# Optimization experiments

Hardware: AMD Instinct MI355X
Metric: run time of the kernel (lower is better)

Reference implementation:

```python
import jax, jax.numpy as jnp
import numpy as np

NUM_HEADS = 16


def setup_inputs() -> dict:
    key = jax.random.key(0)
    ks = jax.random.split(key, 7)
    B, N, D = 16, 512, 1024
    return {
        "x": jax.random.normal(ks[0], (B, N, D), dtype=jnp.float32),
        "spatial_encoding": jax.random.normal(ks[1], (B, N, N), dtype=jnp.float32),
        "edge_encoding": jax.random.normal(ks[2], (B, N, N), dtype=jnp.float32),
        "Wq": jax.random.normal(ks[3], (D, D), dtype=jnp.float32) * (D ** -0.5),
        "Wk": jax.random.normal(ks[4], (D, D), dtype=jnp.float32) * (D ** -0.5),
        "Wv": jax.random.normal(ks[5], (D, D), dtype=jnp.float32) * (D ** -0.5),
        "Wo": jax.random.normal(ks[6], (D, D), dtype=jnp.float32) * (D ** -0.5),
    }


def reference(x, spatial_encoding, edge_encoding, Wq, Wk, Wv, Wo):
    B, N, D = x.shape
    H = NUM_HEADS
    hd = D // H
    scale = D ** -0.5  # NOTE: source scales by hidden_dim**-0.5, not head_size**-0.5

    def split_heads(t):  # (B,N,D) -> (B,H,N,hd)
        return t.reshape(B, N, H, hd).transpose(0, 2, 1, 3)

    q = split_heads(x @ Wq.T)
    k = split_heads(x @ Wk.T)
    v = split_heads(x @ Wv.T)

    bias = (spatial_encoding + edge_encoding)[:, None]  # (B,1,N,N)
    a = jnp.einsum("bhnd,bhmd->bhnm", q, k) * scale + bias  # (B,H,N,N)

    # rows that are entirely zero (padded) are masked to -inf
    row_nonzero = jnp.any(a != 0, axis=-1, keepdims=True)  # (B,H,N,1)
    a = jnp.where(row_nonzero, a, -jnp.inf)
    p = jax.nn.softmax(a, axis=-1)
    p = jnp.where(jnp.isnan(p), 0.0, p)  # nan_to_num after softmax of all -inf rows

    o = jnp.einsum("bhnm,bhmd->bhnd", p, v)  # (B,H,N,hd)
    o = o.transpose(0, 2, 1, 3).reshape(B, N, D)
    return o @ Wo.T
```

## Files before the change

### kernel.cpp

```cpp
#include <hip/hip_runtime.h>
#include <cstdint>


typedef unsigned short u16;
typedef unsigned int   u32;
typedef __attribute__((ext_vector_type(8))) short bf8;
typedef __attribute__((ext_vector_type(4))) float f4;

__device__ __forceinline__ u16 f2bf(float x) {
  u32 u = __float_as_uint(x);
  u += 0x7FFF + ((u >> 16) & 1);
  return (u16)(u >> 16);
}

__device__ __forceinline__ float bf2f(u16 x) {
  return __uint_as_float(((u32)x) << 16);
}

__device__ __forceinline__ void gl2lds16(const void* g, void* l) {
  __builtin_amdgcn_global_load_lds(
      (const __attribute__((address_space(1))) u32*)g,
      (__attribute__((address_space(3))) u32*)l, 16, 0, 0);
}


__global__ __launch_bounds__(256) void cast_bf16(const float* __restrict__ src,
                                                 uint4* __restrict__ dst, int n8) {
  const int i = blockIdx.x * 256 + threadIdx.x;
  if (i >= n8) return;
  const float4* s = (const float4*)src;
  const float4 a = s[2 * i], c = s[2 * i + 1];
  uint4 o;
  o.x = (u32)f2bf(a.x) | ((u32)f2bf(a.y) << 16);
  o.y = (u32)f2bf(a.z) | ((u32)f2bf(a.w) << 16);
  o.z = (u32)f2bf(c.x) | ((u32)f2bf(c.y) << 16);
  o.w = (u32)f2bf(c.z) | ((u32)f2bf(c.w) << 16);
  dst[i] = o;
}

__global__ __launch_bounds__(256) void cast4_bf16(
    const float* __restrict__ s0, const float* __restrict__ s1,
    const float* __restrict__ s2, const float* __restrict__ s3,
    uint4* __restrict__ d0, uint4* __restrict__ d1,
    uint4* __restrict__ d2, uint4* __restrict__ d3) {
  const int i = blockIdx.x * 256 + threadIdx.x;
  const int w = i >> 17, j = i & 131071;
  const float* src = (w == 0) ? s0 : (w == 1) ? s1 : (w == 2) ? s2 : s3;
  uint4* dst = (w == 0) ? d0 : (w == 1) ? d1 : (w == 2) ? d2 : d3;
  const float4* s = (const float4*)src;
  const float4 a = s[2 * j], c = s[2 * j + 1];
  uint4 o;
  o.x = (u32)f2bf(a.x) | ((u32)f2bf(a.y) << 16);
  o.y = (u32)f2bf(a.z) | ((u32)f2bf(a.w) << 16);
  o.z = (u32)f2bf(c.x) | ((u32)f2bf(c.y) << 16);
  o.w = (u32)f2bf(c.z) | ((u32)f2bf(c.w) << 16);
  dst[j] = o;
}

__global__ __launch_bounds__(256) void bias_perm(const float* __restrict__ sp,
                                                 const float* __restrict__ ed,
                                                 u16* __restrict__ Bp) {
  const int jt = blockIdx.x, qt = blockIdx.y, b = blockIdx.z;
  const int tid = threadIdx.x;
  const int wave = tid >> 6, quad = (tid >> 4) & 3, l16 = tid & 15;
  const int qrl = (wave << 4) + (quad << 2);
  union { u16 a[16]; uint4 v[2]; } tmp;
#pragma unroll
  for (int nb = 0; nb < 4; nb++) {
    const int col = (jt << 6) + (nb << 4) + l16;
#pragma unroll
    for (int r = 0; r < 4; r++) {
      const int row = (qt << 6) + qrl + r;
      const size_t idx = ((size_t)b << 18) + (size_t)row * 512 + col;
      tmp.a[nb * 4 + r] = f2bf(sp[idx] + ed[idx]);
    }
  }
  uint4* out = (uint4*)Bp + ((((size_t)b * 8 + qt) * 8 + jt) * 256 + tid) * 2;
  out[0] = tmp.v[0];
  out[1] = tmp.v[1];
}


__device__ __forceinline__ void gemm_core(const u16* __restrict__ A,
                                          const u16* __restrict__ Bt,
                                          int m0, int n0,
                                          u16* lA, u16* lB, f4 acc[4][4]) {
  const int tid  = threadIdx.x;
  const int wave = tid >> 6;
  const int lane = tid & 63;
  const int quad = lane >> 4;
  const int l16  = lane & 15;
  const int wm   = (wave >> 1) << 6;
  const int wn   = (wave & 1) << 6;
  const int srow = tid >> 3;
  const int scol = ((tid & 7) ^ (srow & 7)) << 3;
  const int c0   = (quad ^ (l16 & 7)) << 3;

  f4 zero = {0.f, 0.f, 0.f, 0.f};
#pragma unroll
  for (int mi = 0; mi < 4; mi++)
#pragma unroll
    for (int ni = 0; ni < 4; ni++) acc[mi][ni] = zero;

  const u16* Ab = A  + (size_t)(m0 + srow) * 1024 + scol;
  const u16* Bb = Bt + (size_t)(n0 + srow) * 1024 + scol;

  for (int k0 = 0; k0 < 1024; k0 += 64) {
    __syncthreads();
#pragma unroll
    for (int i = 0; i < 4; i++) {
      gl2lds16(Ab + (size_t)(i << 5) * 1024 + k0,
               (char*)lA + (((i << 8) + (wave << 6)) << 4));
      gl2lds16(Bb + (size_t)(i << 5) * 1024 + k0,
               (char*)lB + (((i << 8) + (wave << 6)) << 4));
    }
    __syncthreads();
#pragma unroll
    for (int kk = 0; kk < 64; kk += 32) {
      const int o = c0 ^ kk;
      bf8 af[4], bfr[4];
#pragma unroll
      for (int mi = 0; mi < 4; mi++)
        af[mi] = *(const bf8*)(lA + (wm + (mi << 4) + l16) * 64 + o);
#pragma unroll
      for (int ni = 0; ni < 4; ni++)
        bfr[ni] = *(const bf8*)(lB + (wn + (ni << 4) + l16) * 64 + o);
#pragma unroll
      for (int mi = 0; mi < 4; mi++)
#pragma unroll
        for (int ni = 0; ni < 4; ni++)
          acc[mi][ni] = __builtin_amdgcn_mfma_f32_16x16x32_bf16(
              af[mi], bfr[ni], acc[mi][ni], 0, 0, 0);
    }
  }
}


__global__ __launch_bounds__(256) void qkv_kernel(
    const u16* __restrict__ xb, const u16* __restrict__ wq,
    const u16* __restrict__ wk, const u16* __restrict__ wv,
    u16* __restrict__ Qh, u16* __restrict__ Kh, u16* __restrict__ Vt) {
  __shared__ __align__(16) u16 lA[128 * 64];
  __shared__ __align__(16) u16 lB[128 * 64];
  const int flat = blockIdx.x + (blockIdx.y << 3) + (blockIdx.z << 9);
  const int m_tile = (flat & 7) | (((flat >> 6) & 7) << 3);
  const int n_tile = (flat >> 3) & 7;
  const int proj = flat >> 9;
  const int m0 = m_tile << 7, n0 = n_tile << 7;
  const u16* W = (proj == 0) ? wq : (proj == 1) ? wk : wv;
  f4 acc[4][4];
  gemm_core(xb, W, m0, n0, lA, lB, acc);

  const int tid = threadIdx.x, wave = tid >> 6, lane = tid & 63;
  const int quad = lane >> 4, l16 = lane & 15;
  const int wm = (wave >> 1) << 6, wn = (wave & 1) << 6;

  if (proj == 2) {
#pragma unroll
    for (int mi = 0; mi < 4; mi++) {
      const int gmb = m0 + wm + (mi << 4) + (quad << 2);
      const int b = gmb >> 9, nb = gmb & 511;
#pragma unroll
      for (int ni = 0; ni < 4; ni++) {
        const int gn = n0 + wn + (ni << 4) + l16;
        const int h = gn >> 6, hdi = gn & 63;
        ushort4 pk;
        pk.x = f2bf(acc[mi][ni][0]);
        pk.y = f2bf(acc[mi][ni][1]);
        pk.z = f2bf(acc[mi][ni][2]);
        pk.w = f2bf(acc[mi][ni][3]);
        *(ushort4*)(Vt + ((size_t)((b << 4) + h) * 64 + hdi) * 512 + nb) = pk;
      }
    }
  } else {
    u16* dst = (proj == 0) ? Qh : Kh;
#pragma unroll
    for (int mi = 0; mi < 4; mi++) {
#pragma unroll
      for (int r = 0; r < 4; r++) {
        const int gm = m0 + wm + (mi << 4) + (quad << 2) + r;
        const int b = gm >> 9, n = gm & 511;
#pragma unroll
        for (int ni = 0; ni < 4; ni++) {
          const int gn = n0 + wn + (ni << 4) + l16;
          const int h = gn >> 6, hdi = gn & 63;
          dst[((size_t)((b << 4) + h) * 512 + n) * 64 + hdi] = f2bf(acc[mi][ni][r]);
        }
      }
    }
  }
}


__global__ __launch_bounds__(256) void oproj_kernel(const u16* __restrict__ Ob,
                                                    const u16* __restrict__ wo,
                                                    float* __restrict__ out) {
  __shared__ __align__(16) u16 lA[128 * 64];
  __shared__ __align__(16) u16 lB[128 * 64];
  const int flat = blockIdx.x + (blockIdx.y << 3);
  const int m0 = ((flat & 7) | (((flat >> 6) & 7) << 3)) << 7;
  const int n0 = ((flat >> 3) & 7) << 7;
  f4 acc[4][4];
  gemm_core(Ob, wo, m0, n0, lA, lB, acc);

  const int tid = threadIdx.x, wave = tid >> 6, lane = tid & 63;
  const int quad = lane >> 4, l16 = lane & 15;
  const int wm = (wave >> 1) << 6, wn = (wave & 1) << 6;
#pragma unroll
  for (int mi = 0; mi < 4; mi++)
#pragma unroll
    for (int r = 0; r < 4; r++) {
      const int gm = m0 + wm + (mi << 4) + (quad << 2) + r;
#pragma unroll
      for (int ni = 0; ni < 4; ni++) {
        const int gn = n0 + wn + (ni << 4) + l16;
        out[(size_t)gm * 1024 + gn] = acc[mi][ni][r];
      }
    }
}


__global__ __launch_bounds__(256) void attn_kernel(
    const u16* __restrict__ Qh, const u16* __restrict__ Kh,
    const u16* __restrict__ Vt, const u16* __restrict__ Bp,
    u16* __restrict__ Ob) {
  __shared__ __align__(16) u16 sQ[64 * 64];
  __shared__ __align__(16) u16 sK[64 * 64];
  __shared__ __align__(16) u16 sV[64 * 64];
  __shared__ __align__(16) u16 sP[4 * 16 * 72];
  const int flat = blockIdx.x + (blockIdx.y << 3) + (blockIdx.z << 7);
  const int qt = (flat >> 3) & 7;
  const int h  = (flat >> 6) & 15;
  const int b  = (flat & 7) | (((flat >> 10) & 1) << 3);
  const int q0 = qt << 6;
  const int tid = threadIdx.x, wave = tid >> 6, lane = tid & 63;
  const int quad = lane >> 4, l16 = lane & 15;
  const int c0  = (quad ^ (l16 & 7)) << 3;
  const int swb = (((tid & 7) ^ ((tid >> 3) & 7)) << 4);

  const u16* Qg = Qh + ((size_t)((b << 4) + h) * 512 + q0) * 64;
  const u16* Kg = Kh + (size_t)((b << 4) + h) * 512 * 64;
  const u16* Vg = Vt + (size_t)((b << 4) + h) * 64 * 512;
  const uint4* Bpg = (const uint4*)Bp + (((size_t)b * 8 + qt) * 8 * 256 + tid) * 2;

#pragma unroll
  for (int i = 0; i < 2; i++) {
    const int e = (i << 8) + tid;
    gl2lds16((const char*)Qg + (e >> 3) * 128 + swb,
             (char*)sQ + (((i << 8) + (wave << 6)) << 4));
  }

  f4 o[4];
  f4 zero = {0.f, 0.f, 0.f, 0.f};
#pragma unroll
  for (int i = 0; i < 4; i++) o[i] = zero;
  float lsum[4] = {0.f, 0.f, 0.f, 0.f};
  const int qrl = (wave << 4) + (quad << 2);

  for (int j0 = 0; j0 < 512; j0 += 64) {
    const uint4 bc0 = Bpg[(j0 >> 6) * 512];
    const uint4 bc1 = Bpg[(j0 >> 6) * 512 + 1];
    const u32 bw[8] = {bc0.x, bc0.y, bc0.z, bc0.w, bc1.x, bc1.y, bc1.z, bc1.w};

    __syncthreads();
#pragma unroll
    for (int i = 0; i < 2; i++) {
      const int e = (i << 8) + tid;
      gl2lds16((const char*)Kg + (size_t)j0 * 128 + (e >> 3) * 128 + swb,
               (char*)sK + (((i << 8) + (wave << 6)) << 4));
      gl2lds16((const char*)Vg + (size_t)(e >> 3) * 1024 + j0 * 2 + swb,
               (char*)sV + (((i << 8) + (wave << 6)) << 4));
    }
    __syncthreads();

    bf8 aq0 = *(const bf8*)(sQ + ((wave << 4) + l16) * 64 + c0);
    bf8 aq1 = *(const bf8*)(sQ + ((wave << 4) + l16) * 64 + (c0 ^ 32));
    u16* pw = sP + wave * (16 * 72);
#pragma unroll
    for (int nb = 0; nb < 4; nb++) {
      bf8 b0 = *(const bf8*)(sK + ((nb << 4) + l16) * 64 + c0);
      bf8 b1 = *(const bf8*)(sK + ((nb << 4) + l16) * 64 + (c0 ^ 32));
      f4 s = zero;
      s = __builtin_amdgcn_mfma_f32_16x16x32_bf16(aq0, b0, s, 0, 0, 0);
      s = __builtin_amdgcn_mfma_f32_16x16x32_bf16(aq1, b1, s, 0, 0, 0);
#pragma unroll
      for (int r = 0; r < 4; r++) {
        const u32 w = bw[nb * 2 + (r >> 1)];
        const float bias = bf2f((r & 1) ? (u16)(w >> 16) : (u16)(w & 0xFFFF));
        const float ev = __expf(s[r] * 0.03125f + bias);
        lsum[r] += ev;
        pw[((quad << 2) + r) * 72 + (nb << 4) + l16] = f2bf(ev);
      }
    }

    bf8 ap0 = *(const bf8*)(pw + l16 * 72 + (quad << 3));
    bf8 ap1 = *(const bf8*)(pw + l16 * 72 + 32 + (quad << 3));
#pragma unroll
    for (int db = 0; db < 4; db++) {
      bf8 v0 = *(const bf8*)(sV + ((db << 4) + l16) * 64 + c0);
      bf8 v1 = *(const bf8*)(sV + ((db << 4) + l16) * 64 + (c0 ^ 32));
      o[db] = __builtin_amdgcn_mfma_f32_16x16x32_bf16(ap0, v0, o[db], 0, 0, 0);
      o[db] = __builtin_amdgcn_mfma_f32_16x16x32_bf16(ap1, v1, o[db], 0, 0, 0);
    }
  }

#pragma unroll
  for (int r = 0; r < 4; r++) {
    float s = lsum[r];
    s += __shfl_xor(s, 1);
    s += __shfl_xor(s, 2);
    s += __shfl_xor(s, 4);
    s += __shfl_xor(s, 8);
    const float inv = 1.f / s;
    const int gr = q0 + qrl + r;
#pragma unroll
    for (int db = 0; db < 4; db++)
      Ob[(size_t)((b << 9) + gr) * 1024 + (h << 6) + (db << 4) + l16] =
          f2bf(o[db][r] * inv);
  }
}


extern "C" void kernel_launch(void* const* d_in, const int* in_sizes, int n_in,
                              void* d_out, int out_size, void* d_ws, size_t ws_size,
                              hipStream_t stream) {
  const float* x  = (const float*)d_in[0];
  const float* sp = (const float*)d_in[1];
  const float* ed = (const float*)d_in[2];
  const float* Wq = (const float*)d_in[3];
  const float* Wk = (const float*)d_in[4];
  const float* Wv = (const float*)d_in[5];
  const float* Wo = (const float*)d_in[6];
  float* out = (float*)d_out;

  char* w = (char*)d_ws;
  u16* xb  = (u16*)(w);
  u16* wqb = (u16*)(w + 16777216);
  u16* wkb = (u16*)(w + 18874368);
  u16* wvb = (u16*)(w + 20971520);
  u16* wob = (u16*)(w + 23068672);
  u16* Qh  = (u16*)(w + 25165824);
  u16* Kh  = (u16*)(w + 41943040);
  u16* Vt  = (u16*)(w + 58720256);
  u16* Ob  = (u16*)(w + 75497472);
  u16* Bp  = (u16*)(w + 92274688);

  cast_bf16<<<4096, 256, 0, stream>>>(x, (uint4*)xb, 1048576);
  cast4_bf16<<<2048, 256, 0, stream>>>(Wq, Wk, Wv, Wo,
                                       (uint4*)wqb, (uint4*)wkb,
                                       (uint4*)wvb, (uint4*)wob);
  bias_perm<<<dim3(8, 8, 16), 256, 0, stream>>>(sp, ed, Bp);

  qkv_kernel<<<dim3(8, 64, 3), 256, 0, stream>>>(xb, wqb, wkb, wvb, Qh, Kh, Vt);
  attn_kernel<<<dim3(8, 16, 16), 256, 0, stream>>>(Qh, Kh, Vt, Bp, Ob);
  oproj_kernel<<<dim3(8, 64, 1), 256, 0, stream>>>(Ob, wob, out);
}
```

Measured before the change: 251.7 us.

## Keep softmax probabilities in registers via transposed QK^T and fp16 PV MFMA

The attention kernel now computes S^T (K as the A operand, Q as B) so that each lane's exp values directly form the B operand of a 16x16x16 fp16 MFMA for P·V. This removes the per-wave LDS staging buffer for P and its write/read round trip. V is now stored as fp16 instead of bf16 so the PV MFMA can use fp16 inputs. The bias permutation is changed to match the transposed layout. The three prep kernels are merged into one launch. The fp16 P and V trade range for mantissa precision, and the PV product now issues more, smaller MFMAs.

```diff
diff --git a/kernel.cpp b/kernel.cpp
--- a/kernel.cpp
+++ b/kernel.cpp
@@ -5,6 +5,7 @@
 typedef unsigned short u16;
 typedef unsigned int   u32;
 typedef __attribute__((ext_vector_type(8))) short bf8;
+typedef __attribute__((ext_vector_type(4))) _Float16 h4;
 typedef __attribute__((ext_vector_type(4))) float f4;
 
 __device__ __forceinline__ u16 f2bf(float x) {
@@ -17,6 +18,12 @@
   return __uint_as_float(((u32)x) << 16);
 }
 
+__device__ __forceinline__ u16 f2h(float x) {
+  union { _Float16 h; u16 u; } c;
+  c.h = (_Float16)x;
+  return c.u;
+}
+
 __device__ __forceinline__ void gl2lds16(const void* g, void* l) {
   __builtin_amdgcn_global_load_lds(
       (const __attribute__((address_space(1))) u32*)g,
@@ -24,60 +31,57 @@
 }
 
 
-__global__ __launch_bounds__(256) void cast_bf16(const float* __restrict__ src,
-                                                 uint4* __restrict__ dst, int n8) {
-  const int i = blockIdx.x * 256 + threadIdx.x;
-  if (i >= n8) return;
-  const float4* s = (const float4*)src;
-  const float4 a = s[2 * i], c = s[2 * i + 1];
-  uint4 o;
-  o.x = (u32)f2bf(a.x) | ((u32)f2bf(a.y) << 16);
-  o.y = (u32)f2bf(a.z) | ((u32)f2bf(a.w) << 16);
-  o.z = (u32)f2bf(c.x) | ((u32)f2bf(c.y) << 16);
-  o.w = (u32)f2bf(c.z) | ((u32)f2bf(c.w) << 16);
-  dst[i] = o;
-}
-
-__global__ __launch_bounds__(256) void cast4_bf16(
-    const float* __restrict__ s0, const float* __restrict__ s1,
-    const float* __restrict__ s2, const float* __restrict__ s3,
+__global__ __launch_bounds__(256) void prep_kernel(
+    const float* __restrict__ x, const float* __restrict__ sp,
+    const float* __restrict__ ed,
+    const float* __restrict__ W0, const float* __restrict__ W1,
+    const float* __restrict__ W2, const float* __restrict__ W3,
+    uint4* __restrict__ xb,
     uint4* __restrict__ d0, uint4* __restrict__ d1,
-    uint4* __restrict__ d2, uint4* __restrict__ d3) {
-  const int i = blockIdx.x * 256 + threadIdx.x;
-  const int w = i >> 17, j = i & 131071;
-  const float* src = (w == 0) ? s0 : (w == 1) ? s1 : (w == 2) ? s2 : s3;
-  uint4* dst = (w == 0) ? d0 : (w == 1) ? d1 : (w == 2) ? d2 : d3;
-  const float4* s = (const float4*)src;
-  const float4 a = s[2 * j], c = s[2 * j + 1];
-  uint4 o;
-  o.x = (u32)f2bf(a.x) | ((u32)f2bf(a.y) << 16);
-  o.y = (u32)f2bf(a.z) | ((u32)f2bf(a.w) << 16);
-  o.z = (u32)f2bf(c.x) | ((u32)f2bf(c.y) << 16);
-  o.w = (u32)f2bf(c.z) | ((u32)f2bf(c.w) << 16);
-  dst[j] = o;
-}
-
-__global__ __launch_bounds__(256) void bias_perm(const float* __restrict__ sp,
-                                                 const float* __restrict__ ed,
-                                                 u16* __restrict__ Bp) {
-  const int jt = blockIdx.x, qt = blockIdx.y, b = blockIdx.z;
+    uint4* __restrict__ d2, uint4* __restrict__ d3,
+    u16* __restrict__ Bp) {
+  const int bid = blockIdx.x;
   const int tid = threadIdx.x;
-  const int wave = tid >> 6, quad = (tid >> 4) & 3, l16 = tid & 15;
-  const int qrl = (wave << 4) + (quad << 2);
-  union { u16 a[16]; uint4 v[2]; } tmp;
-#pragma unroll
-  for (int nb = 0; nb < 4; nb++) {
-    const int col = (jt << 6) + (nb << 4) + l16;
-#pragma unroll
-    for (int r = 0; r < 4; r++) {
-      const int row = (qt << 6) + qrl + r;
-      const size_t idx = ((size_t)b << 18) + (size_t)row * 512 + col;
-      tmp.a[nb * 4 + r] = f2bf(sp[idx] + ed[idx]);
-    }
-  }
-  uint4* out = (uint4*)Bp + ((((size_t)b * 8 + qt) * 8 + jt) * 256 + tid) * 2;
-  out[0] = tmp.v[0];
-  out[1] = tmp.v[1];
+  if (bid < 6144) {
+    const float* src;
+    uint4* dst;
+    int j;
+    if (bid < 4096) {
+      src = x; dst = xb; j = bid * 256 + tid;
+    } else {
+      const int i = (bid - 4096) * 256 + tid;
+      const int w = i >> 17;
+      j = i & 131071;
+      src = (w == 0) ? W0 : (w == 1) ? W1 : (w == 2) ? W2 : W3;
+      dst = (w == 0) ? d0 : (w == 1) ? d1 : (w == 2) ? d2 : d3;
+    }
+    const float4* s = (const float4*)src;
+    const float4 a = s[2 * j], c = s[2 * j + 1];
+    uint4 o;
+    o.x = (u32)f2bf(a.x) | ((u32)f2bf(a.y) << 16);
+    o.y = (u32)f2bf(a.z) | ((u32)f2bf(a.w) << 16);
+    o.z = (u32)f2bf(c.x) | ((u32)f2bf(c.y) << 16);
+    o.w = (u32)f2bf(c.z) | ((u32)f2bf(c.w) << 16);
+    dst[j] = o;
+  } else {
+    const int id = bid - 6144;
+    const int jt = id & 7, qt = (id >> 3) & 7, b = id >> 6;
+    const int wave = tid >> 6, quad = (tid >> 4) & 3, l16 = tid & 15;
+    const int row = (qt << 6) + (wave << 4) + l16;
+    union { u16 a[16]; uint4 v[2]; } tmp;
+#pragma unroll
+    for (int jb = 0; jb < 4; jb++) {
+#pragma unroll
+      for (int r = 0; r < 4; r++) {
+        const int col = (jt << 6) + (jb << 4) + (quad << 2) + r;
+        const size_t idx = ((size_t)b << 18) + (size_t)row * 512 + col;
+        tmp.a[jb * 4 + r] = f2bf(sp[idx] + ed[idx]);
+      }
+    }
+    uint4* out = (uint4*)Bp + ((((size_t)b * 8 + qt) * 8 + jt) * 256 + tid) * 2;
+    out[0] = tmp.v[0];
+    out[1] = tmp.v[1];
+  }
 }
 
 
@@ -165,10 +169,10 @@
         const int gn = n0 + wn + (ni << 4) + l16;
         const int h = gn >> 6, hdi = gn & 63;
         ushort4 pk;
-        pk.x = f2bf(acc[mi][ni][0]);
-        pk.y = f2bf(acc[mi][ni][1]);
-        pk.z = f2bf(acc[mi][ni][2]);
-        pk.w = f2bf(acc[mi][ni][3]);
+        pk.x = f2h(acc[mi][ni][0]);
+        pk.y = f2h(acc[mi][ni][1]);
+        pk.z = f2h(acc[mi][ni][2]);
+        pk.w = f2h(acc[mi][ni][3]);
         *(ushort4*)(Vt + ((size_t)((b << 4) + h) * 64 + hdi) * 512 + nb) = pk;
       }
     }
@@ -227,7 +231,6 @@
   __shared__ __align__(16) u16 sQ[64 * 64];
   __shared__ __align__(16) u16 sK[64 * 64];
   __shared__ __align__(16) u16 sV[64 * 64];
-  __shared__ __align__(16) u16 sP[4 * 16 * 72];
   const int flat = blockIdx.x + (blockIdx.y << 3) + (blockIdx.z << 7);
   const int qt = (flat >> 3) & 7;
   const int h  = (flat >> 6) & 15;
@@ -249,13 +252,15 @@
     gl2lds16((const char*)Qg + (e >> 3) * 128 + swb,
              (char*)sQ + (((i << 8) + (wave << 6)) << 4));
   }
+  __syncthreads();
+  const bf8 bq0 = *(const bf8*)(sQ + ((wave << 4) + l16) * 64 + c0);
+  const bf8 bq1 = *(const bf8*)(sQ + ((wave << 4) + l16) * 64 + (c0 ^ 32));
 
   f4 o[4];
   f4 zero = {0.f, 0.f, 0.f, 0.f};
 #pragma unroll
   for (int i = 0; i < 4; i++) o[i] = zero;
-  float lsum[4] = {0.f, 0.f, 0.f, 0.f};
-  const int qrl = (wave << 4) + (quad << 2);
+  float lsum = 0.f;
 
   for (int j0 = 0; j0 < 512; j0 += 64) {
     const uint4 bc0 = Bpg[(j0 >> 6) * 512];
@@ -273,50 +278,49 @@
     }
     __syncthreads();
 
-    bf8 aq0 = *(const bf8*)(sQ + ((wave << 4) + l16) * 64 + c0);
-    bf8 aq1 = *(const bf8*)(sQ + ((wave << 4) + l16) * 64 + (c0 ^ 32));
-    u16* pw = sP + wave * (16 * 72);
-#pragma unroll
-    for (int nb = 0; nb < 4; nb++) {
-      bf8 b0 = *(const bf8*)(sK + ((nb << 4) + l16) * 64 + c0);
-      bf8 b1 = *(const bf8*)(sK + ((nb << 4) + l16) * 64 + (c0 ^ 32));
+    h4 pf[4];
+#pragma unroll
+    for (int jb = 0; jb < 4; jb++) {
+      bf8 a0 = *(const bf8*)(sK + ((jb << 4) + l16) * 64 + c0);
+      bf8 a1 = *(const bf8*)(sK + ((jb << 4) + l16) * 64 + (c0 ^ 32));
       f4 s = zero;
-      s = __builtin_amdgcn_mfma_f32_16x16x32_bf16(aq0, b0, s, 0, 0, 0);
-      s = __builtin_amdgcn_mfma_f32_16x16x32_bf16(aq1, b1, s, 0, 0, 0);
+      s = __builtin_amdgcn_mfma_f32_16x16x32_bf16(a0, bq0, s, 0, 0, 0);
+      s = __builtin_amdgcn_mfma_f32_16x16x32_bf16(a1, bq1, s, 0, 0, 0);
 #pragma unroll
       for (int r = 0; r < 4; r++) {
-        const u32 w = bw[nb * 2 + (r >> 1)];
+        const u32 w = bw[jb * 2 + (r >> 1)];
         const float bias = bf2f((r & 1) ? (u16)(w >> 16) : (u16)(w & 0xFFFF));
         const float ev = __expf(s[r] * 0.03125f + bias);
-        lsum[r] += ev;
-        pw[((quad << 2) + r) * 72 + (nb << 4) + l16] = f2bf(ev);
-      }
-    }
-
-    bf8 ap0 = *(const bf8*)(pw + l16 * 72 + (quad << 3));
-    bf8 ap1 = *(const bf8*)(pw + l16 * 72 + 32 + (quad << 3));
+        lsum += ev;
+        pf[jb][r] = (_Float16)ev;
+      }
+    }
+
 #pragma unroll
     for (int db = 0; db < 4; db++) {
-      bf8 v0 = *(const bf8*)(sV + ((db << 4) + l16) * 64 + c0);
-      bf8 v1 = *(const bf8*)(sV + ((db << 4) + l16) * 64 + (c0 ^ 32));
-      o[db] = __builtin_amdgcn_mfma_f32_16x16x32_bf16(ap0, v0, o[db], 0, 0, 0);
-      o[db] = __builtin_amdgcn_mfma_f32_16x16x32_bf16(ap1, v1, o[db], 0, 0, 0);
-    }
-  }
-
-#pragma unroll
-  for (int r = 0; r < 4; r++) {
-    float s = lsum[r];
-    s += __shfl_xor(s, 1);
-    s += __shfl_xor(s, 2);
-    s += __shfl_xor(s, 4);
-    s += __shfl_xor(s, 8);
-    const float inv = 1.f / s;
-    const int gr = q0 + qrl + r;
-#pragma unroll
-    for (int db = 0; db < 4; db++)
-      Ob[(size_t)((b << 9) + gr) * 1024 + (h << 6) + (db << 4) + l16] =
-          f2bf(o[db][r] * inv);
+#pragma unroll
+      for (int jb = 0; jb < 4; jb++) {
+        const h4 va = *(const h4*)(sV + ((db << 4) + l16) * 64 +
+                                   ((((jb << 1) + (quad >> 1)) ^ (l16 & 7)) << 3) +
+                                   ((quad & 1) << 2));
+        o[db] = __builtin_amdgcn_mfma_f32_16x16x16f16(va, pf[jb], o[db], 0, 0, 0);
+      }
+    }
+  }
+
+  lsum += __shfl_xor(lsum, 16);
+  lsum += __shfl_xor(lsum, 32);
+  const float inv = 1.f / lsum;
+  const int q = q0 + (wave << 4) + l16;
+#pragma unroll
+  for (int db = 0; db < 4; db++) {
+    ushort4 pk;
+    pk.x = f2bf(o[db][0] * inv);
+    pk.y = f2bf(o[db][1] * inv);
+    pk.z = f2bf(o[db][2] * inv);
+    pk.w = f2bf(o[db][3] * inv);
+    *(ushort4*)(Ob + (size_t)((b << 9) + q) * 1024 + (h << 6) + (db << 4) +
+                (quad << 2)) = pk;
   }
 }
 
@@ -345,12 +349,9 @@
   u16* Ob  = (u16*)(w + 75497472);
   u16* Bp  = (u16*)(w + 92274688);
 
-  cast_bf16<<<4096, 256, 0, stream>>>(x, (uint4*)xb, 1048576);
-  cast4_bf16<<<2048, 256, 0, stream>>>(Wq, Wk, Wv, Wo,
-                                       (uint4*)wqb, (uint4*)wkb,
-                                       (uint4*)wvb, (uint4*)wob);
-  bias_perm<<<dim3(8, 8, 16), 256, 0, stream>>>(sp, ed, Bp);
-
+  prep_kernel<<<7168, 256, 0, stream>>>(x, sp, ed, Wq, Wk, Wv, Wo,
+                                        (uint4*)xb, (uint4*)wqb, (uint4*)wkb,
+                                        (uint4*)wvb, (uint4*)wob, Bp);
   qkv_kernel<<<dim3(8, 64, 3), 256, 0, stream>>>(xb, wqb, wkb, wvb, Qh, Kh, Vt);
   attn_kernel<<<dim3(8, 16, 16), 256, 0, stream>>>(Qh, Kh, Vt, Bp, Ob);
   oproj_kernel<<<dim3(8, 64, 1), 256, 0, stream>>>(Ob, wob, out);
```

After: 252.1 us. About the same (+0.2%).
